# Optimization experiments

Measured on AMD Instinct MI355X. Metric: run time of the kernel, lower is better.

Reference implementation:

```python
import jax, jax.numpy as jnp
import numpy as np

N = 100000
E = 1600000
N_IN = 512
N_H = 128


def setup_inputs() -> dict:
    key = jax.random.key(0)
    ks = jax.random.split(key, 8)
    x = jax.random.normal(ks[0], (N, N_IN), dtype=jnp.float32)
    src = jax.random.randint(ks[1], (E,), 0, N, dtype=jnp.int32)
    dst = jax.random.randint(ks[2], (E,), 0, N, dtype=jnp.int32)
    perm = jax.random.permutation(ks[3], N).astype(jnp.int32)
    # GraphConv params (in_feats=512 -> out_feats=128), xavier-ish scale
    W = jax.random.normal(ks[4], (N_IN, N_H), dtype=jnp.float32) / np.sqrt(N_IN)
    b = jnp.zeros((N_H,), dtype=jnp.float32)
    alpha = jnp.full((N_H,), 0.25, dtype=jnp.float32)  # PReLU(n_h) init
    mlp_W = jax.random.normal(ks[5], (N_H, N_H), dtype=jnp.float32) / np.sqrt(N_H)
    mlp_b = jnp.zeros((N_H,), dtype=jnp.float32)
    return {"x": x, "src": src, "dst": dst, "perm": perm, "W": W, "b": b,
            "alpha": alpha, "mlp_W": mlp_W, "mlp_b": mlp_b, "batch_train": 0}


def _degree_norm(idx, n):
    deg = jax.ops.segment_sum(jnp.ones_like(idx, dtype=jnp.float32), idx, num_segments=n)
    return jnp.clip(deg, 1.0, None) ** -0.5  # [n]


def _gcn_layer(x, src, dst, W, b, alpha):
    n = x.shape[0]
    norm_out = _degree_norm(src, n)  # src-side out-degree norm
    norm_in = _degree_norm(dst, n)   # dst-side in-degree norm
    # in_feats > out_feats: apply weight first (DGL GraphConv ordering)
    h = x @ W                                  # [N, n_h]
    h = h * norm_out[:, None]
    agg = jax.ops.segment_sum(h[src], dst, num_segments=n)  # SpMM copy_u/sum
    agg = agg * norm_in[:, None] + b
    return jnp.where(agg >= 0, agg, alpha * agg)  # PReLU(n_h)


def reference(x, src, dst, perm, W, b, alpha, mlp_W, mlp_b, batch_train):
    z1 = _gcn_layer(x, src, dst, W, b, alpha)          # clean encoder
    z2 = _gcn_layer(x[perm], src, dst, W, b, alpha)    # corrupted encoder
    z1 = z1 @ mlp_W + mlp_b
    z2 = z2 @ mlp_W + mlp_b
    logit = jnp.concatenate((z1.sum(1), z2.sum(1)), axis=0)  # [2N]
    return logit
```

## Files before the change

### kernel.cpp

```cpp
#include <hip/hip_runtime.h>


typedef __bf16 bf16x8 __attribute__((ext_vector_type(8)));
typedef float f32x4 __attribute__((ext_vector_type(4)));

#define PAD 48
#define NBMAX 256
#define EPB 4096

__device__ inline unsigned short f2bf(float f) {
  unsigned u = __float_as_uint(f);
  u += 0x7fffu + ((u >> 16) & 1u);
  return (unsigned short)(u >> 16);
}
__device__ inline float2 bfpair(unsigned u) {
  float2 r;
  r.x = __uint_as_float(u << 16);
  r.y = __uint_as_float(u & 0xffff0000u);
  return r;
}

__device__ __forceinline__ void gld16(const void* g, void* l) {
  __builtin_amdgcn_global_load_lds(
      (const __attribute__((address_space(1))) void*)g,
      (__attribute__((address_space(3))) void*)l, 16, 0, 0);
}

__global__ __launch_bounds__(256) void k_bin(const int* __restrict__ src,
                                             const int* __restrict__ dst,
                                             int* __restrict__ gCntD,
                                             int* __restrict__ gCntS,
                                             int* __restrict__ dstbin,
                                             unsigned short* __restrict__ srcbin,
                                             int E, int NB, int CAP) {
  __shared__ int2 stage[EPB];
  __shared__ int cntD[NBMAX], cntS[NBMAX], baseD[NBMAX], baseS[NBMAX];
  const int tid = threadIdx.x;
  const int e0 = blockIdx.x * EPB;
  const int nloc = min(EPB, E - e0);

  for (int b = tid; b < NB; b += 256) { cntD[b] = 0; cntS[b] = 0; }
  __syncthreads();

#pragma unroll
  for (int it = 0; it < EPB / 256; ++it) {
    int i = it * 256 + tid;
    if (i < nloc) {
      int s = src[e0 + i];
      int d = dst[e0 + i];
      stage[i] = make_int2(s, d);
      atomicAdd(&cntD[d >> 9], 1);
      atomicAdd(&cntS[s >> 9], 1);
    }
  }
  __syncthreads();

  for (int b = tid; b < NB; b += 256) {
    baseD[b] = atomicAdd(&gCntD[b], cntD[b]);
    baseS[b] = atomicAdd(&gCntS[b], cntS[b]);
    cntD[b] = 0;
    cntS[b] = 0;
  }
  __syncthreads();

#pragma unroll
  for (int it = 0; it < EPB / 256; ++it) {
    int i = it * 256 + tid;
    if (i < nloc) {
      int2 sd = stage[i];
      int s = sd.x, d = sd.y;
      int bd = d >> 9;
      int p = atomicAdd(&cntD[bd], 1) + baseD[bd];
      if (p < CAP) dstbin[(size_t)bd * CAP + p] = (s << 9) | (d & 511);
      int bs = s >> 9;
      int q = atomicAdd(&cntS[bs], 1) + baseS[bs];
      if (q < CAP) srcbin[(size_t)bs * CAP + q] = (unsigned short)(s & 511);
    }
  }
}

__global__ __launch_bounds__(256) void k_csr(const int* __restrict__ gCntD,
                                             const int* __restrict__ dstbin,
                                             int* __restrict__ col,
                                             int* __restrict__ deg_d,
                                             float* __restrict__ norm_i,
                                             int N, int CAP) {
  __shared__ int cnt[512];
  const int b = blockIdx.x;
  const int tid = threadIdx.x;
  cnt[tid] = 0;
  cnt[tid + 256] = 0;
  __syncthreads();
  int cb = gCntD[b];
  if (cb > CAP) cb = CAP;
  const int* bin = dstbin + (size_t)b * CAP;
  for (int i = tid; i < cb; i += 256) {
    int rec = bin[i];
    int d9 = rec & 511;
    int s = rec >> 9;
    int pos = atomicAdd(&cnt[d9], 1);
    if (pos < PAD) col[((size_t)b * 512 + d9) * PAD + pos] = s;
  }
  __syncthreads();
  for (int t = tid; t < 512; t += 256) {
    int i = b * 512 + t;
    if (i < N) {
      int c = cnt[t];
      deg_d[i] = (c > PAD) ? PAD : c;
      norm_i[i] = rsqrtf((float)((c < 1) ? 1 : c));
    }
  }
}

__global__ __launch_bounds__(256) void k_shist(const int* __restrict__ gCntS,
                                               const unsigned short* __restrict__ srcbin,
                                               const int* __restrict__ perm,
                                               float* __restrict__ norm_o,
                                               int* __restrict__ inv,
                                               int N, int CAP) {
  __shared__ int hist[512];
  const int b = blockIdx.x;
  const int tid = threadIdx.x;
  hist[tid] = 0;
  hist[tid + 256] = 0;
  __syncthreads();
  int cb = gCntS[b];
  if (cb > CAP) cb = CAP;
  const unsigned short* bin = srcbin + (size_t)b * CAP;
  for (int i = tid; i < cb; i += 256) {
    atomicAdd(&hist[bin[i]], 1);
  }
  __syncthreads();
  for (int t = tid; t < 512; t += 256) {
    int i = b * 512 + t;
    if (i < N) {
      int h = hist[t];
      norm_o[i] = rsqrtf((float)((h < 1) ? 1 : h));
      inv[perm[i]] = i;
    }
  }
}

__global__ __launch_bounds__(256) void k_fill_dev(const int* __restrict__ src,
                                                  const int* __restrict__ dst,
                                                  int* __restrict__ deg_s,
                                                  int* __restrict__ cnt,
                                                  int* __restrict__ col, int E) {
  int t = blockIdx.x * 256 + threadIdx.x;
  int e0 = t * 4;
  if (e0 >= E) return;
  int e1 = (e0 + 4 < E) ? e0 + 4 : E;
  for (int e = e0; e < e1; e++) {
    int s = src[e], d = dst[e];
    atomicAdd(&deg_s[s], 1);
    int pos = atomicAdd(&cnt[d], 1);
    if (pos < PAD) col[(size_t)d * PAD + pos] = s;
  }
}

__global__ __launch_bounds__(256) void k_finish_dev(const int* __restrict__ deg_s,
                                                    const int* __restrict__ cnt,
                                                    const int* __restrict__ perm,
                                                    float* __restrict__ norm_o,
                                                    float* __restrict__ norm_i,
                                                    int* __restrict__ deg_d,
                                                    int* __restrict__ inv, int N) {
  int i = blockIdx.x * 256 + threadIdx.x;
  if (i >= N) return;
  int a = deg_s[i]; if (a < 1) a = 1;
  int b = cnt[i];
  deg_d[i] = (b > PAD) ? PAD : b;
  if (b < 1) b = 1;
  norm_o[i] = rsqrtf((float)a);
  norm_i[i] = rsqrtf((float)b);
  inv[perm[i]] = i;
}

__global__ __launch_bounds__(256) void k_castw(const float* __restrict__ W,
                                               unsigned short* __restrict__ WT) {
  int i = blockIdx.x * 256 + threadIdx.x;
  int k = i >> 7;
  int n = i & 127;
  WT[n * 512 + k] = f2bf(W[i]);
}

__global__ __launch_bounds__(256) void k_gemm(const float* __restrict__ X,
                                              const unsigned short* __restrict__ WT,
                                              const float* __restrict__ norm_o,
                                              const int* __restrict__ inv,
                                              unsigned short* __restrict__ HH, int M) {
  __shared__ __align__(16) unsigned char lds_raw[32768];
  float* Asf = (float*)lds_raw;
  unsigned short* Bsh = (unsigned short*)(lds_raw + 16384);
  unsigned short* smem = (unsigned short*)lds_raw;

  const int tid = threadIdx.x;
  const int wave = tid >> 6;
  const int lane = tid & 63;
  const int m = lane & 15;
  const int quad = lane >> 4;
  const int block_row = blockIdx.x * 64;

  f32x4 acc[8];
#pragma unroll
  for (int t = 0; t < 8; t++) acc[t] = (f32x4){0.f, 0.f, 0.f, 0.f};

  const int ar0 = tid >> 3, as0 = (tid & 7) ^ (ar0 & 7);
  const int g1 = 256 + tid;
  const int ar1 = g1 >> 3, as1 = (g1 & 7) ^ (ar1 & 7);
  int gra0 = block_row + ar0; if (gra0 >= M) gra0 = M - 1;
  int gra1 = block_row + ar1; if (gra1 >= M) gra1 = M - 1;
  const float* srcA0 = X + (size_t)gra0 * 512 + as0 * 4;
  const float* srcA1 = X + (size_t)gra1 * 512 + as1 * 4;
  const int bn0 = tid >> 2, bs0 = tid & 3;
  const int bn1 = g1 >> 2, bs1 = g1 & 3;
  const unsigned short* srcB0 = WT + (size_t)bn0 * 512 + bs0 * 8;
  const unsigned short* srcB1 = WT + (size_t)bn1 * 512 + bs1 * 8;

  auto stage = [&](int buf, int kt) {
    const int k0 = kt * 32;
    float* la = Asf + buf * 2048;
    unsigned short* lb = Bsh + buf * 4096;
    gld16(srcA0 + k0, la + tid * 4);
    gld16(srcA1 + k0, la + g1 * 4);
    gld16(srcB0 + k0, lb + tid * 8);
    gld16(srcB1 + k0, lb + g1 * 8);
  };

  stage(0, 0);
  __syncthreads();

  const int r = wave * 16 + m;
  const int sl0 = ((quad * 2) ^ (r & 7)) * 4;
  const int sl1 = ((quad * 2 + 1) ^ (r & 7)) * 4;

  int cur = 0;
  for (int kt = 0; kt < 16; ++kt) {
    if (kt < 15) stage(cur ^ 1, kt + 1);
    const float* Ab = Asf + cur * 2048;
    const unsigned short* Bb = Bsh + cur * 4096;
    f32x4 a0 = *(const f32x4*)(Ab + r * 32 + sl0);
    f32x4 a1 = *(const f32x4*)(Ab + r * 32 + sl1);
    union { bf16x8 v; __bf16 h[8]; } au;
#pragma unroll
    for (int j = 0; j < 4; ++j) {
      au.h[j] = (__bf16)a0[j];
      au.h[4 + j] = (__bf16)a1[j];
    }
#pragma unroll
    for (int t = 0; t < 8; ++t) {
      bf16x8 b = *(const bf16x8*)(Bb + (t * 16 + m) * 32 + quad * 8);
      acc[t] = __builtin_amdgcn_mfma_f32_16x16x32_bf16(au.v, b, acc[t], 0, 0, 0);
    }
    __syncthreads();
    cur ^= 1;
  }

  float no1[4], no2[4];
#pragma unroll
  for (int rr4 = 0; rr4 < 4; rr4++) {
    int rr = block_row + wave * 16 + quad * 4 + rr4;
    no1[rr4] = 0.f;
    no2[rr4] = 0.f;
    if (rr < M) {
      no1[rr4] = norm_o[rr];
      no2[rr4] = norm_o[inv[rr]];
    }
  }

#pragma unroll
  for (int t = 0; t < 8; t++) {
    int c = t * 16 + m;
#pragma unroll
    for (int rr4 = 0; rr4 < 4; rr4++) {
      int row = wave * 16 + quad * 4 + rr4;
      smem[row * 128 + c] = f2bf(acc[t][rr4] * no1[rr4]);
    }
  }
  __syncthreads();
#pragma unroll
  for (int it = 0; it < 4; it++) {
    int idx = tid + it * 256;
    int row = idx >> 4;
    int c8 = (idx & 15) * 8;
    int gr = block_row + row;
    if (gr < M)
      *(int4*)(HH + (size_t)gr * 256 + c8) = *(int4*)&smem[row * 128 + c8];
  }
  __syncthreads();

#pragma unroll
  for (int t = 0; t < 8; t++) {
    int c = t * 16 + m;
#pragma unroll
    for (int rr4 = 0; rr4 < 4; rr4++) {
      int row = wave * 16 + quad * 4 + rr4;
      smem[row * 128 + c] = f2bf(acc[t][rr4] * no2[rr4]);
    }
  }
  __syncthreads();
#pragma unroll
  for (int it = 0; it < 4; it++) {
    int idx = tid + it * 256;
    int row = idx >> 4;
    int c8 = (idx & 15) * 8;
    int gr = block_row + row;
    if (gr < M) {
      int q = inv[gr];
      *(int4*)(HH + (size_t)q * 256 + 128 + c8) = *(int4*)&smem[row * 128 + c8];
    }
  }
}

__global__ __launch_bounds__(128) void k_wsum(const float* __restrict__ mlpW,
                                              const float* __restrict__ mlpb,
                                              float* __restrict__ wsum,
                                              float* __restrict__ bsum) {
  __shared__ float sb[128];
  int k = threadIdx.x;
  float s = 0.f;
  for (int j = 0; j < 128; j++) s += mlpW[k * 128 + j];
  wsum[k] = s;
  sb[k] = mlpb[k];
  __syncthreads();
  for (int off = 64; off > 0; off >>= 1) {
    if (k < off) sb[k] += sb[k + off];
    __syncthreads();
  }
  if (k == 0) bsum[0] = sb[0];
}

__global__ __launch_bounds__(256) void k_agg(const unsigned short* __restrict__ HH,
                                             const int* __restrict__ deg_d,
                                             const int* __restrict__ col,
                                             const float* __restrict__ norm_i,
                                             const float* __restrict__ bias,
                                             const float* __restrict__ alpha,
                                             const float* __restrict__ wsum,
                                             const float* __restrict__ bsum,
                                             float* __restrict__ out, int N) {
  int wave = (blockIdx.x * 256 + threadIdx.x) >> 6;
  int lane = threadIdx.x & 63;
  if (wave >= N) return;
  const int g = lane >> 4;
  const int sl = lane & 15;

  int cl = deg_d[wave];
  const int* cbase = col + (size_t)wave * PAD;

  float a1[8], a2[8];
#pragma unroll
  for (int i = 0; i < 8; i++) { a1[i] = 0.f; a2[i] = 0.f; }

  for (int j0 = 0; j0 < cl; j0 += 4) {
    int j = j0 + g;
    int je = (j < cl) ? j : cl - 1;
    int s = cbase[je];
    float mk = (j < cl) ? 1.f : 0.f;
    const unsigned short* rp = HH + (size_t)s * 256 + sl * 8;
    int4 r1 = *(const int4*)rp;
    int4 r2 = *(const int4*)(rp + 128);
    const unsigned* u1 = (const unsigned*)&r1;
    const unsigned* u2 = (const unsigned*)&r2;
#pragma unroll
    for (int q = 0; q < 4; q++) {
      float2 v1 = bfpair(u1[q]);
      float2 v2 = bfpair(u2[q]);
      a1[2 * q]     = fmaf(v1.x, mk, a1[2 * q]);
      a1[2 * q + 1] = fmaf(v1.y, mk, a1[2 * q + 1]);
      a2[2 * q]     = fmaf(v2.x, mk, a2[2 * q]);
      a2[2 * q + 1] = fmaf(v2.y, mk, a2[2 * q + 1]);
    }
  }

#pragma unroll
  for (int i = 0; i < 8; i++) {
    a1[i] += __shfl_xor(a1[i], 16);
    a1[i] += __shfl_xor(a1[i], 32);
    a2[i] += __shfl_xor(a2[i], 16);
    a2[i] += __shfl_xor(a2[i], 32);
  }

  float ni = norm_i[wave];
  float4 bb0 = ((const float4*)bias)[sl * 2];
  float4 bb1 = ((const float4*)bias)[sl * 2 + 1];
  float4 al0 = ((const float4*)alpha)[sl * 2];
  float4 al1 = ((const float4*)alpha)[sl * 2 + 1];
  float4 ws0 = ((const float4*)wsum)[sl * 2];
  float4 ws1 = ((const float4*)wsum)[sl * 2 + 1];
  float bs = bsum[0];
  float bb[8] = {bb0.x, bb0.y, bb0.z, bb0.w, bb1.x, bb1.y, bb1.z, bb1.w};
  float al[8] = {al0.x, al0.y, al0.z, al0.w, al1.x, al1.y, al1.z, al1.w};
  float wsv[8] = {ws0.x, ws0.y, ws0.z, ws0.w, ws1.x, ws1.y, ws1.z, ws1.w};

  float p1 = 0.f, p2 = 0.f;
#pragma unroll
  for (int i = 0; i < 8; i++) {
    float g1 = a1[i] * ni + bb[i];
    float g2 = a2[i] * ni + bb[i];
    g1 = (g1 >= 0.f) ? g1 : al[i] * g1;
    g2 = (g2 >= 0.f) ? g2 : al[i] * g2;
    p1 = fmaf(g1, wsv[i], p1);
    p2 = fmaf(g2, wsv[i], p2);
  }
#pragma unroll
  for (int off = 8; off > 0; off >>= 1) {
    p1 += __shfl_down(p1, off);
    p2 += __shfl_down(p2, off);
  }
  if (lane == 0) {
    out[wave] = p1 + bs;
    out[N + wave] = p2 + bs;
  }
}


extern "C" void kernel_launch(void* const* d_in, const int* in_sizes, int n_in,
                              void* d_out, int out_size, void* d_ws, size_t ws_size,
                              hipStream_t stream) {
  const float* x = (const float*)d_in[0];
  const int* src = (const int*)d_in[1];
  const int* dst = (const int*)d_in[2];
  const int* perm = (const int*)d_in[3];
  const float* W = (const float*)d_in[4];
  const float* bias = (const float*)d_in[5];
  const float* alpha = (const float*)d_in[6];
  const float* mlpW = (const float*)d_in[7];
  const float* mlpb = (const float*)d_in[8];

  const int E = in_sizes[1];
  const int N = in_sizes[3];
  float* out = (float*)d_out;

  char* ws = (char*)d_ws;
  size_t off = 0;
  auto alloc = [&](size_t bytes) -> void* {
    void* p = ws + off;
    off = (off + bytes + 255) & ~(size_t)255;
    return p;
  };

  unsigned short* HH = (unsigned short*)alloc((size_t)N * 256 * sizeof(unsigned short));
  int* col = (int*)alloc((size_t)N * PAD * sizeof(int));
  unsigned short* WT = (unsigned short*)alloc(512 * 128 * sizeof(unsigned short));
  float* norm_o = (float*)alloc((size_t)N * sizeof(float));
  float* norm_i = (float*)alloc((size_t)N * sizeof(float));
  int* inv = (int*)alloc((size_t)N * sizeof(int));
  int* deg_d = (int*)alloc((size_t)N * sizeof(int));
  float* wsum = (float*)alloc(512);
  float* bsum = (float*)alloc(256);
  size_t common = off;

  const int NB = (N + 511) >> 9;
  const int meanB = (NB > 0) ? E / NB : 0;
  const int CAP = ((meanB * 5) / 4 + 1023) & ~1023;

  size_t need_binned = common + (size_t)NB * CAP * sizeof(int) +
                       (size_t)NB * CAP * sizeof(unsigned short) +
                       2 * (size_t)NBMAX * sizeof(int) + 4096;
  bool binned = (NB <= NBMAX) && ((ws_size == 0) || (ws_size >= need_binned));

  const int nbN = (N + 255) / 256;
  const int nbE4 = ((E + 3) / 4 + 255) / 256;

  k_castw<<<512 * 128 / 256, 256, 0, stream>>>(W, WT);
  k_wsum<<<1, 128, 0, stream>>>(mlpW, mlpb, wsum, bsum);

  if (binned) {
    int* dstbin = (int*)alloc((size_t)NB * CAP * sizeof(int));
    unsigned short* srcbin = (unsigned short*)alloc((size_t)NB * CAP * sizeof(unsigned short));
    int* gCntD = (int*)alloc((size_t)NBMAX * sizeof(int));
    int* gCntS = (int*)alloc((size_t)NBMAX * sizeof(int));
    hipMemsetAsync(gCntD, 0, (size_t)NBMAX * sizeof(int), stream);
    hipMemsetAsync(gCntS, 0, (size_t)NBMAX * sizeof(int), stream);
    const int nbBin = (E + EPB - 1) / EPB;
    k_bin<<<nbBin, 256, 0, stream>>>(src, dst, gCntD, gCntS, dstbin, srcbin,
                                     E, NB, CAP);
    k_csr<<<NB, 256, 0, stream>>>(gCntD, dstbin, col, deg_d, norm_i, N, CAP);
    k_shist<<<NB, 256, 0, stream>>>(gCntS, srcbin, perm, norm_o, inv, N, CAP);
  } else {
    int* deg_s = (int*)alloc((size_t)N * sizeof(int));
    int* cnt = (int*)alloc((size_t)N * sizeof(int));
    hipMemsetAsync(deg_s, 0, (size_t)N * sizeof(int), stream);
    hipMemsetAsync(cnt, 0, (size_t)N * sizeof(int), stream);
    k_fill_dev<<<nbE4, 256, 0, stream>>>(src, dst, deg_s, cnt, col, E);
    k_finish_dev<<<nbN, 256, 0, stream>>>(deg_s, cnt, perm, norm_o, norm_i,
                                          deg_d, inv, N);
  }

  k_gemm<<<(N + 63) / 64, 256, 0, stream>>>(x, WT, norm_o, inv, HH, N);
  k_agg<<<(N + 3) / 4, 256, 0, stream>>>(HH, deg_d, col, norm_i,
                                         bias, alpha, wsum, bsum, out, N);
}
```

Baseline: 514.2 us.

## Deepen GEMM prefetch pipeline, swizzle B tile in LDS, batch gather loads in SpMM

The GEMM loop now issues two stages ahead and waits with explicit vmcnt counts and raw barriers instead of __syncthreads, so global-to-LDS loads for the next tiles overlap compute. The B tile is XOR-swizzled in LDS to reduce bank conflicts on the MFMA operand reads. The aggregation kernel unrolls the neighbor gather four-wide, issuing four edges' row loads before accumulating to raise memory-level parallelism. The cost is more register pressure and fragile hand-placed wait counts.

```diff
diff --git a/kernel.cpp b/kernel.cpp
--- a/kernel.cpp
+++ b/kernel.cpp
@@ -212,8 +212,8 @@
   int gra1 = block_row + ar1; if (gra1 >= M) gra1 = M - 1;
   const float* srcA0 = X + (size_t)gra0 * 512 + as0 * 4;
   const float* srcA1 = X + (size_t)gra1 * 512 + as1 * 4;
-  const int bn0 = tid >> 2, bs0 = tid & 3;
-  const int bn1 = g1 >> 2, bs1 = g1 & 3;
+  const int bn0 = tid >> 2, bs0 = (tid & 3) ^ ((bn0 >> 1) & 3);
+  const int bn1 = g1 >> 2, bs1 = (g1 & 3) ^ ((bn1 >> 1) & 3);
   const unsigned short* srcB0 = WT + (size_t)bn0 * 512 + bs0 * 8;
   const unsigned short* srcB1 = WT + (size_t)bn1 * 512 + bs1 * 8;
 
@@ -228,15 +228,22 @@
   };
 
   stage(0, 0);
-  __syncthreads();
+  stage(1, 1);
 
   const int r = wave * 16 + m;
   const int sl0 = ((quad * 2) ^ (r & 7)) * 4;
   const int sl1 = ((quad * 2 + 1) ^ (r & 7)) * 4;
 
   int cur = 0;
+#pragma unroll
   for (int kt = 0; kt < 16; ++kt) {
-    if (kt < 15) stage(cur ^ 1, kt + 1);
+    if (kt < 15) {
+      asm volatile("s_waitcnt vmcnt(4)" ::: "memory");
+    } else {
+      asm volatile("s_waitcnt vmcnt(0)" ::: "memory");
+    }
+    __builtin_amdgcn_s_barrier();
+    __builtin_amdgcn_sched_barrier(0);
     const float* Ab = Asf + cur * 2048;
     const unsigned short* Bb = Bsh + cur * 4096;
     f32x4 a0 = *(const f32x4*)(Ab + r * 32 + sl0);
@@ -249,10 +256,14 @@
     }
 #pragma unroll
     for (int t = 0; t < 8; ++t) {
-      bf16x8 b = *(const bf16x8*)(Bb + (t * 16 + m) * 32 + quad * 8);
+      int R = t * 16 + m;
+      int bslot = quad ^ ((R >> 1) & 3);
+      bf16x8 b = *(const bf16x8*)(Bb + R * 32 + bslot * 8);
       acc[t] = __builtin_amdgcn_mfma_f32_16x16x32_bf16(au.v, b, acc[t], 0, 0, 0);
     }
-    __syncthreads();
+    __builtin_amdgcn_sched_barrier(0);
+    __builtin_amdgcn_s_barrier();
+    if (kt < 14) stage(cur, kt + 2);
     cur ^= 1;
   }
 
@@ -352,24 +363,32 @@
 #pragma unroll
   for (int i = 0; i < 8; i++) { a1[i] = 0.f; a2[i] = 0.f; }
 
-  for (int j0 = 0; j0 < cl; j0 += 4) {
-    int j = j0 + g;
-    int je = (j < cl) ? j : cl - 1;
-    int s = cbase[je];
-    float mk = (j < cl) ? 1.f : 0.f;
-    const unsigned short* rp = HH + (size_t)s * 256 + sl * 8;
-    int4 r1 = *(const int4*)rp;
-    int4 r2 = *(const int4*)(rp + 128);
-    const unsigned* u1 = (const unsigned*)&r1;
-    const unsigned* u2 = (const unsigned*)&r2;
-#pragma unroll
-    for (int q = 0; q < 4; q++) {
-      float2 v1 = bfpair(u1[q]);
-      float2 v2 = bfpair(u2[q]);
-      a1[2 * q]     = fmaf(v1.x, mk, a1[2 * q]);
-      a1[2 * q + 1] = fmaf(v1.y, mk, a1[2 * q + 1]);
-      a2[2 * q]     = fmaf(v2.x, mk, a2[2 * q]);
-      a2[2 * q + 1] = fmaf(v2.y, mk, a2[2 * q + 1]);
+  for (int j0 = 0; j0 < cl; j0 += 16) {
+    int4 r1[4], r2[4];
+    float mk[4];
+#pragma unroll
+    for (int u = 0; u < 4; ++u) {
+      int j = j0 + u * 4 + g;
+      int je = (j < cl) ? j : cl - 1;
+      int s = cbase[je];
+      mk[u] = (j < cl) ? 1.f : 0.f;
+      const unsigned short* rp = HH + (size_t)s * 256 + sl * 8;
+      r1[u] = *(const int4*)rp;
+      r2[u] = *(const int4*)(rp + 128);
+    }
+#pragma unroll
+    for (int u = 0; u < 4; ++u) {
+      const unsigned* u1 = (const unsigned*)&r1[u];
+      const unsigned* u2 = (const unsigned*)&r2[u];
+#pragma unroll
+      for (int q = 0; q < 4; q++) {
+        float2 v1 = bfpair(u1[q]);
+        float2 v2 = bfpair(u2[q]);
+        a1[2 * q]     = fmaf(v1.x, mk[u], a1[2 * q]);
+        a1[2 * q + 1] = fmaf(v1.y, mk[u], a1[2 * q + 1]);
+        a2[2 * q]     = fmaf(v2.x, mk[u], a2[2 * q]);
+        a2[2 * q + 1] = fmaf(v2.y, mk[u], a2[2 * q + 1]);
+      }
     }
   }
 
```

Result: no change. 511.7 us (-0.5%).
